# Optimization experiments

Hardware: AMD Instinct MI355X
Metric: run time of the kernel (lower is better)

The kernel has to match this reference:

```python
import jax, jax.numpy as jnp
import numpy as np
from jax import lax

BITS = 8

def dec2bin(q, bits=BITS):
    # q: integer-valued float tensor (NCHW or OIHW); stack two's-complement bit-planes along axis 1
    u = jnp.mod(jnp.round(q).astype(jnp.int32), 2 ** bits)
    return jnp.concatenate([((u >> k) & 1) for k in range(bits)], axis=1).astype(jnp.float32)

def quant_sym(x, bits=BITS):
    # brevitas-style signed symmetric per-tensor fake-quant (zero_point = 0)
    n = 2.0 ** (bits - 1) - 1.0
    scale = jnp.max(jnp.abs(x)) / n
    q = jnp.clip(jnp.round(x / scale), -n, n)  # q == value/scale + zero_point
    return q * scale, q

def quant_relu(x, bits=BITS):
    # QuantReLU: unsigned per-tensor fake-quant after relu
    r = jnp.maximum(x, 0.0)
    n = 2.0 ** bits - 1.0
    scale = jnp.max(r) / n
    q = jnp.clip(jnp.round(r / scale), 0.0, n)
    return q * scale, q

def conv(x, w, stride, pad):
    return lax.conv_general_dilated(x, w, (stride, stride), [(pad, pad), (pad, pad)],
                                    dimension_numbers=('NCHW', 'OIHW', 'NCHW'))

def bn(x, g, b, m, v, eps=1e-5):
    inv = g * lax.rsqrt(v + eps)
    return x * inv[None, :, None, None] + (b - m * inv)[None, :, None, None]

def setup_inputs() -> dict:
    key = jax.random.key(0)
    ks = jax.random.split(key, 11)
    N, C, H, W = 16, 64, 56, 56
    return {
        'x':  jax.random.normal(ks[0], (N, C, H, W), jnp.float32),
        'w1': jax.random.normal(ks[1], (C, C, 3, 3), jnp.float32) * 0.05,
        'w2': jax.random.normal(ks[2], (C, C, 3, 3), jnp.float32) * 0.05,
        'g1': jax.random.uniform(ks[3], (C,), jnp.float32, 0.5, 1.5),
        'b1': jax.random.normal(ks[4], (C,), jnp.float32) * 0.1,
        'm1': jax.random.normal(ks[5], (C,), jnp.float32) * 0.1,
        'v1': jax.random.uniform(ks[6], (C,), jnp.float32, 0.5, 1.5),
        'g2': jax.random.uniform(ks[7], (C,), jnp.float32, 0.5, 1.5),
        'b2': jax.random.normal(ks[8], (C,), jnp.float32) * 0.1,
        'm2': jax.random.normal(ks[9], (C,), jnp.float32) * 0.1,
        'v2': jax.random.uniform(ks[10], (C,), jnp.float32, 0.5, 1.5),
    }

def reference(x, w1, w2, g1, b1, m1, v1, g2, b2, m2, v2):
    stride = 1
    # quant_input (QuantIdentity) produces the quant tensor entering the block
    xq, qx = quant_sym(x)
    identity = xq
    # HM_activation: total number of set bits in the int activation
    HM_act = jnp.sum(dec2bin(qx))
    # HM_energy: L1 norm of conv over bit-decomposed int activations/weights
    w1q, qw1 = quant_sym(w1)
    HM_energy = jnp.sum(jnp.abs(conv(dec2bin(qx), dec2bin(qw1), stride, 1)))
    # conv1 -> bn1 -> QuantReLU
    o = bn(conv(xq, w1q, stride, 1), g1, b1, m1, v1)
    o1, q1 = quant_relu(o)
    HM_act = HM_act + jnp.sum(dec2bin(q1))
    w2q, qw2 = quant_sym(w2)
    HM_energy = HM_energy + jnp.sum(jnp.abs(conv(dec2bin(q1), dec2bin(qw2), 1, 1)))
    # conv2 -> bn2 -> residual add -> QuantReLU
    o = bn(conv(o1, w2q, 1, 1), g2, b2, m2, v2)
    o = o + identity
    out, _ = quant_relu(o)
    return out, HM_act, HM_energy
```

## Files before the change

kernel.cpp:

```cpp
#include <hip/hip_runtime.h>

using u32 = unsigned int;
typedef int v4i __attribute__((ext_vector_type(4)));

constexpr int N_IMG   = 16;
constexpr int PADROW  = 4096;
constexpr int ROWS_PI = 58;

constexpr size_t OFS_QX   = 4096;
constexpr size_t SZ_QPAD  = (size_t)(1 + N_IMG * ROWS_PI) * PADROW;
constexpr size_t OFS_Q1   = OFS_QX + SZ_QPAD;
constexpr size_t OFS_O1   = OFS_Q1 + SZ_QPAD;
constexpr size_t SZ_OF    = (size_t)N_IMG * 56 * 56 * 64 * 4;
constexpr size_t OFS_O2   = OFS_O1 + SZ_OF;
constexpr size_t OFS_QW1  = OFS_O2 + SZ_OF;
constexpr size_t OFS_QW2  = OFS_QW1 + 36864;
constexpr size_t OFS_WB1  = OFS_QW2 + 36864;
constexpr size_t OFS_WB2  = OFS_WB1 + 18432;
constexpr size_t OFS_WSUM = OFS_WB2 + 18432;
constexpr size_t OFS_SCAL = OFS_WSUM + 256;
constexpr size_t OFS_STX  = OFS_SCAL + 384;
constexpr size_t OFS_STQ  = OFS_STX + 18432;
constexpr size_t OFS_WSRED= OFS_STQ + 18432;
constexpr size_t WS_NEED  = OFS_WSRED + 4096;
constexpr size_t ZSPAN    = OFS_WSRED - OFS_WSUM;
constexpr size_t OUTN     = (size_t)16 * 64 * 56 * 56;

static __device__ __forceinline__ float block_redmax(float v, float* red, int t) {
    red[t] = v; __syncthreads();
    for (int s = 128; s > 0; s >>= 1) {
        if (t < s) red[t] = fmaxf(red[t], red[t + s]);
        __syncthreads();
    }
    float r = red[0]; __syncthreads();
    return r;
}

__global__ __launch_bounds__(256) void k_absmax_qw(const float* __restrict__ x,
                                                   const float* __restrict__ w1,
                                                   const float* __restrict__ w2,
                                                   char* __restrict__ qw1, char* __restrict__ qw2,
                                                   int* __restrict__ wb1, int* __restrict__ wb2,
                                                   int* __restrict__ wsum, float* __restrict__ scal,
                                                   float* __restrict__ wsred) {
    __shared__ union { float red[256]; int wsl[256]; } sm;
    int b = blockIdx.x, t = threadIdx.x;
    if (b < 1024) {
        float mx = 0.f;
        const float4* p4 = (const float4*)x;
        for (int i = b * 256 + t; i < 802816; i += 1024 * 256) {
            float4 v = p4[i];
            mx = fmaxf(mx, fmaxf(fmaxf(fabsf(v.x), fabsf(v.y)),
                                 fmaxf(fabsf(v.z), fabsf(v.w))));
        }
        mx = block_redmax(mx, sm.red, t);
        if (t == 0) wsred[b] = mx;
        return;
    }
    int wu = b - 1024;
    int wsel = wu / 9, kp = wu - wsel * 9;
    const float* w = wsel ? w2 : w1;
    char* qw = wsel ? qw2 : qw1;
    int* wb  = wsel ? wb2 : wb1;
    float mx = 0.f;
    const float4* p4 = (const float4*)w;
    for (int i = t; i < 9216; i += 256) {
        float4 v = p4[i];
        mx = fmaxf(mx, fmaxf(fmaxf(fabsf(v.x), fabsf(v.y)),
                             fmaxf(fabsf(v.z), fabsf(v.w))));
    }
    float maxW = block_redmax(mx, sm.red, t);
    if (t == 0 && kp == 0) scal[1 + wsel] = maxW;
    float s = maxW / 127.f;
    int co = t & 63, cg = t >> 6, ci0 = cg * 16;
    signed char qv[16];
    int qsum = 0;
#pragma unroll
    for (int i = 0; i < 16; i++) {
        int ci = ci0 + i;
        float v = w[((size_t)co * 64 + ci) * 9 + kp];
        float qf = rintf(v / s);
        qf = fminf(fmaxf(qf, -127.f), 127.f);
        int q = (int)qf;
        qv[i] = (signed char)q;
        qsum += q;
    }
    u32 pk[4];
#pragma unroll
    for (int d = 0; d < 4; d++)
        pk[d] = ((u32)(unsigned char)qv[d*4]) | ((u32)(unsigned char)qv[d*4+1] << 8)
              | ((u32)(unsigned char)qv[d*4+2] << 16) | ((u32)(unsigned char)qv[d*4+3] << 24);
    *(uint4*)&qw[(size_t)(kp * 64 + co) * 64 + ci0] = *(uint4*)pk;
#pragma unroll
    for (int i = 0; i < 16; i++) {
        u32 uu = (u32)(unsigned char)qv[i];
#pragma unroll
        for (int k = 0; k < 8; k++) {
            unsigned long long bal = __ballot((uu >> k) & 1);
            if (co == 0) wb[((ci0 + i) * 8 + k) * 9 + kp] = __popcll(bal);
        }
    }
    if (wsel == 1) {
        __syncthreads();
        sm.wsl[t] = qsum; __syncthreads();
        if (t < 64)
            atomicAdd(&wsum[t], sm.wsl[t] + sm.wsl[t + 64] + sm.wsl[t + 128] + sm.wsl[t + 192]);
    }
}

__global__ __launch_bounds__(256) void k_quant_x(const float* __restrict__ x,
                                                 char* __restrict__ qpad,
                                                 const float* __restrict__ wsred,
                                                 float* __restrict__ scal) {
    __shared__ union { float red[256]; char lq[4096]; } sm;
    int n = blockIdx.x, yy = blockIdx.y, t = threadIdx.x;
    u32* row = (u32*)(qpad + (size_t)(1 + n * ROWS_PI + yy) * PADROW);
    if (n == 0 && yy == 0) {
        u32* r0 = (u32*)qpad;
        for (int j = t; j < 1024; j += 256) r0[j] = 0u;
    }
    if (yy == 0 || yy == 57) {
        for (int j = t; j < 1024; j += 256) row[j] = 0u;
        return;
    }
    float a = fmaxf(fmaxf(wsred[t], wsred[t + 256]),
                    fmaxf(wsred[t + 512], wsred[t + 768]));
    float maxX = block_redmax(a, sm.red, t);
    if (n == 0 && yy == 1 && t == 0) scal[0] = maxX;
    int y = yy - 1;
    float sxq = maxX / 127.f;
    const float4* xr = (const float4*)(x + (size_t)n * 200704 + (size_t)y * 56);
    for (int j = t; j < 896; j += 256) {
        int c = j / 14, xq = j - c * 14;
        float4 v = xr[(size_t)c * 784 + xq];
#pragma unroll
        for (int i = 0; i < 4; i++) {
            float q = rintf(((const float*)&v)[i] / sxq);
            q = fminf(fmaxf(q, -127.f), 127.f);
            sm.lq[(4 * xq + i) * 64 + c] = (char)(int)q;
        }
    }
    __syncthreads();
    u32* lqd = (u32*)sm.lq;
    for (int j = t; j < 1024; j += 256) row[j] = (j < 896) ? lqd[j] : 0u;
}

static __device__ __forceinline__ void unpack_acc(u32 v, u32 pk[8]) {
#pragma unroll
    for (int k = 0; k < 8; k++) pk[k] += (v >> k) & 0x01010101u;
}

static __device__ __forceinline__ void reduce_cat(u32* red, int* gdst, const u32 pk[8],
                                                  bool active, int t) {
#pragma unroll
    for (int k = 0; k < 8; k++) red[t * 9 + k] = active ? pk[k] : 0u;
    __syncthreads();
#pragma unroll
    for (int p = t; p < 512; p += 256) {
        int ci = p >> 3, k = p & 7, ci4 = ci >> 2, bb = ci & 3;
        int sum = 0;
#pragma unroll
        for (int xo = 0; xo < 16; xo++)
            sum += (red[(xo * 16 + ci4) * 9 + k] >> (8 * bb)) & 0xFF;
        if (sum) atomicAdd(&gdst[p], sum);
    }
    __syncthreads();
}

template <int FROMF>
static __device__ __forceinline__ u32 pk_at(const u32* img, const float* ofb, float s1,
                                            u32 xm, int row, int xx, int ci4) {
    if (FROMF) {
        float4 v = *(const float4*)(ofb + (size_t)row * 3584 + xx * 64 + ci4 * 4);
        u32 pk = 0;
#pragma unroll
        for (int i = 0; i < 4; i++) {
            float vv = fmaxf(((const float*)&v)[i], 0.f);
            u32 q = (u32)(int)fminf(rintf(vv / s1), 255.f);
            pk |= q << (8 * i);
        }
        return pk;
    }
    return img[(size_t)row * 1024 + xx * 16 + ci4] ^ xm;
}

template <int FROMF>
static __device__ void stats_unit(u32* red, const char* qpad, const float* of, float s1,
                                  u32 xorm, int* gst, int s, int t) {
    int n = s >> 3, slab = s & 7;
    int ci4 = t & 15, xo = t >> 4;
    const u32* img = FROMF ? nullptr : (const u32*)(qpad + (size_t)(2 + n * ROWS_PI) * PADROW);
    const float* ofb = FROMF ? (of + (size_t)n * 56 * 3584) : nullptr;
    u32 xm = xorm * 0x01010101u;
    int y0 = slab * 7;
    {
        u32 pk[8] = {0,0,0,0,0,0,0,0};
#pragma unroll
        for (int r = 0; r < 7; r++)
#pragma unroll
            for (int j = 0; j < 4; j++) {
                int xx = xo + 16 * j;
                if (xx < 56) unpack_acc(pk_at<FROMF>(img, ofb, s1, xm, y0 + r, xx, ci4), pk);
            }
        reduce_cat(red, gst + 0 * 512, pk, true, t);
    }
    {
        u32 pk[8] = {0,0,0,0,0,0,0,0};
        bool act = (xo == 0);
        if (act)
#pragma unroll
            for (int r = 0; r < 7; r++)
                unpack_acc(pk_at<FROMF>(img, ofb, s1, xm, y0 + r, 0, ci4), pk);
        reduce_cat(red, gst + 3 * 512, pk, act, t);
    }
    {
        u32 pk[8] = {0,0,0,0,0,0,0,0};
        bool act = (xo == 7);
        if (act)
#pragma unroll
            for (int r = 0; r < 7; r++)
                unpack_acc(pk_at<FROMF>(img, ofb, s1, xm, y0 + r, 55, ci4), pk);
        reduce_cat(red, gst + 4 * 512, pk, act, t);
    }
    if (slab == 0) {
        u32 pk[8] = {0,0,0,0,0,0,0,0};
#pragma unroll
        for (int j = 0; j < 4; j++) {
            int xx = xo + 16 * j;
            if (xx < 56) unpack_acc(pk_at<FROMF>(img, ofb, s1, xm, 0, xx, ci4), pk);
        }
        reduce_cat(red, gst + 1 * 512, pk, true, t);
        if (t < 32) {
            int which = t >> 4, c4 = t & 15;
            u32 v = pk_at<FROMF>(img, ofb, s1, xm, 0, which ? 55 : 0, c4);
            for (int b = 0; b < 4; b++)
                for (int k = 0; k < 8; k++)
                    if ((v >> (8 * b + k)) & 1)
                        atomicAdd(&gst[(5 + which) * 512 + (c4 * 4 + b) * 8 + k], 1);
        }
    }
    if (slab == 7) {
        u32 pk[8] = {0,0,0,0,0,0,0,0};
#pragma unroll
        for (int j = 0; j < 4; j++) {
            int xx = xo + 16 * j;
            if (xx < 56) unpack_acc(pk_at<FROMF>(img, ofb, s1, xm, 55, xx, ci4), pk);
        }
        reduce_cat(red, gst + 2 * 512, pk, true, t);
        if (t < 32) {
            int which = t >> 4, c4 = t & 15;
            u32 v = pk_at<FROMF>(img, ofb, s1, xm, 55, which ? 55 : 0, c4);
            for (int b = 0; b < 4; b++)
                for (int k = 0; k < 8; k++)
                    if ((v >> (8 * b + k)) & 1)
                        atomicAdd(&gst[(7 + which) * 512 + (c4 * 4 + b) * 8 + k], 1);
        }
    }
}

template <int SECOND>
__global__ __launch_bounds__(256, 2) void k_conv(const char* __restrict__ qin,
                                                 const char* __restrict__ qw,
                                                 const int* __restrict__ wsum,
                                                 const char* __restrict__ qid,
                                                 const float* __restrict__ gg, const float* __restrict__ bb,
                                                 const float* __restrict__ mmp, const float* __restrict__ vvp,
                                                 const float* __restrict__ scal,
                                                 float* __restrict__ outp, u32* __restrict__ rmaxp) {
    __shared__ __align__(16) u32 lb[11520];
    __shared__ __align__(16) u32 lin[3960];
    __shared__ float red[4];
    int b = blockIdx.x, t = threadIdx.x;
    int w = t >> 6, lane = t & 63, mq = lane & 15, quad = lane >> 4;
    int u0 = b * 2;
    int n = u0 / 56, y = u0 - n * 56;
    const uint4* bq4 = (const uint4*)qw;
    for (int j4 = t; j4 < 2304; j4 += 256) {
        int r_ = j4 >> 2, rem = j4 & 3;
        *(uint4*)&lb[r_ * 20 + rem * 4] = bq4[j4];
    }
    const uint4* qin4 = (const uint4*)qin;
    size_t pbase = (size_t)(1 + n * ROWS_PI + y) * 256;
    for (int r4 = t; r4 < 792; r4 += 256) {
        int ky = r4 / 264, r = r4 - ky * 264;
        int px = r >> 2, rem = r & 3;
        *(uint4*)&lin[(ky * 66 + px) * 20 + rem * 4] = qin4[pbase + (size_t)ky * 256 - 4 + r];
    }
    float sIn = SECOND ? __uint_as_float(((const u32*)scal)[32]) / 255.f : scal[0] / 127.f;
    float sW  = scal[1 + SECOND] / 127.f;
    float sx  = scal[0] / 127.f;
    float alpha[4], beta[4]; int wofs[4];
#pragma unroll
    for (int nt = 0; nt < 4; nt++) {
        int co = nt * 16 + mq;
        float inv = gg[co] * rsqrtf(vvp[co] + 1e-5f);
        alpha[nt] = sIn * sW * inv;
        beta[nt]  = bb[co] - mmp[co] * inv;
        wofs[nt]  = SECOND ? (wsum[co] << 7) : 0;
    }
    __syncthreads();
    float lmax = 0.f;
#pragma unroll
    for (int rr = 0; rr < 2; rr++) {
        if (rr == 1) {
            __syncthreads();
            for (int r4 = t; r4 < 264; r4 += 256) {
                int px = r4 >> 2, rem = r4 & 3;
                *(uint4*)&lin[px * 20 + rem * 4] = qin4[pbase + 3 * 256 - 4 + r4];
            }
            __syncthreads();
        }
        v4i acc[4] = {{0,0,0,0},{0,0,0,0},{0,0,0,0},{0,0,0,0}};
#pragma unroll
        for (int ky = 0; ky < 3; ky++) {
            int slot = (ky + rr) % 3;
#pragma unroll
            for (int kx = 0; kx < 3; kx++) {
                int px = w * 16 + mq + kx;
                v4i a = *(const v4i*)&lin[(slot * 66 + px) * 20 + quad * 4];
                int tap = ky * 3 + kx;
#pragma unroll
                for (int nt = 0; nt < 4; nt++) {
                    int co = nt * 16 + mq;
                    v4i bf = *(const v4i*)&lb[(tap * 64 + co) * 20 + quad * 4];
                    acc[nt] = __builtin_amdgcn_mfma_i32_16x16x64_i8(a, bf, acc[nt], 0, 0, 0);
                }
            }
        }
        int uu = u0 + rr, yr = y + rr;
        size_t rowb = (size_t)uu * 3584;
        const signed char* idrow = SECOND
            ? (const signed char*)(qid + (size_t)(2 + n * ROWS_PI + yr) * PADROW) : nullptr;
#pragma unroll
        for (int nt = 0; nt < 4; nt++) {
            int co = nt * 16 + mq;
#pragma unroll
            for (int r = 0; r < 4; r++) {
                int xx = w * 16 + quad * 4 + r;
                if (xx < 56) {
                    float o = (float)(acc[nt][r] + wofs[nt]) * alpha[nt] + beta[nt];
                    if (SECOND) o += sx * (float)idrow[xx * 64 + co];
                    outp[rowb + xx * 64 + co] = o;
                    lmax = fmaxf(lmax, o);
                }
            }
        }
    }
#pragma unroll
    for (int off = 32; off > 0; off >>= 1) lmax = fmaxf(lmax, __shfl_down(lmax, off));
    if (lane == 0) red[w] = lmax;
    __syncthreads();
    if (t == 0)
        atomicMax(rmaxp, __float_as_uint(fmaxf(fmaxf(red[0], red[1]), fmaxf(red[2], red[3]))));
}

__global__ __launch_bounds__(256) void k_qrelu1(const float* __restrict__ o1,
                                                char* __restrict__ q1,
                                                const char* __restrict__ qx,
                                                const float* __restrict__ scal,
                                                int* __restrict__ stx, int* __restrict__ stq) {
    __shared__ u32 sred[2304];
    int b = blockIdx.x, t = threadIdx.x;
    if (b >= 1056) {
        float s1 = __uint_as_float(((const u32*)scal)[32]) / 255.f;
        stats_unit<1>(sred, nullptr, o1, s1, 0u, stq, b - 1056, t);
        return;
    }
    if (b >= 928) { stats_unit<0>(sred, qx, nullptr, 0.f, 0u, stx, b - 928, t); return; }
    int n = b / 58, yy = b - n * 58;
    u32* row = (u32*)(q1 + (size_t)(1 + n * ROWS_PI + yy) * PADROW);
    if (n == 0 && yy == 0) {
        u32* r0 = (u32*)q1;
        for (int j = t; j < 1024; j += 256) r0[j] = 0x80808080u;
    }
    if (yy == 0 || yy == 57) {
        for (int j = t; j < 1024; j += 256) row[j] = 0x80808080u;
        return;
    }
    int y = yy - 1;
    float s1 = __uint_as_float(((const u32*)scal)[32]) / 255.f;
    const float4* o4 = (const float4*)(o1 + (size_t)(n * 56 + y) * 3584);
    for (int j = t; j < 1024; j += 256) {
        u32 pk = 0x80808080u;
        if (j < 896) {
            float4 v = o4[j];
            pk = 0u;
#pragma unroll
            for (int i = 0; i < 4; i++) {
                float vv = fmaxf(((const float*)&v)[i], 0.f);
                float q = fminf(rintf(vv / s1), 255.f);
                pk |= ((u32)(unsigned char)(char)((int)q - 128)) << (8 * i);
            }
        }
        row[j] = pk;
    }
}

__global__ __launch_bounds__(256) void k_final(const float* __restrict__ o2,
                                               const float* __restrict__ scal,
                                               float* __restrict__ outp,
                                               const int* __restrict__ stx, const int* __restrict__ stq,
                                               const int* __restrict__ wb1, const int* __restrict__ wb2) {
    __shared__ union { float lt[64 * 57]; long long r1[256]; } sm;
    int b = blockIdx.x, t = threadIdx.x;
    if (b == 448) {
        long long act = 0, en = 0;
#pragma unroll
        for (int half = 0; half < 2; half++) {
            int tt = t + half * 256;
#pragma unroll
            for (int wsel = 0; wsel < 2; wsel++) {
                const int* st = wsel ? stq : stx;
                const int* wb = wsel ? wb2 : wb1;
                long long s[9];
#pragma unroll
                for (int j = 0; j < 9; j++) s[j] = st[j * 512 + tt];
                int wr[9];
#pragma unroll
                for (int j = 0; j < 9; j++) wr[j] = wb[tt * 9 + j];
                long long wall = 0;
#pragma unroll
                for (int j = 0; j < 9; j++) wall += wr[j];
                long long wr0 = (long long)wr[0] + wr[1] + wr[2];
                long long wr2 = (long long)wr[6] + wr[7] + wr[8];
                long long wc0 = (long long)wr[0] + wr[3] + wr[6];
                long long wc2 = (long long)wr[2] + wr[5] + wr[8];
                en += s[0] * wall - s[1] * wr2 - s[2] * wr0 - s[3] * wc2 - s[4] * wc0
                    + s[5] * (long long)wr[8] + s[6] * (long long)wr[6]
                    + s[7] * (long long)wr[2] + s[8] * (long long)wr[0];
                act += s[0];
            }
        }
        sm.r1[t] = en; __syncthreads();
        for (int s = 128; s > 0; s >>= 1) { if (t < s) sm.r1[t] += sm.r1[t + s]; __syncthreads(); }
        long long etot = sm.r1[0]; __syncthreads();
        sm.r1[t] = act; __syncthreads();
        for (int s = 128; s > 0; s >>= 1) { if (t < s) sm.r1[t] += sm.r1[t + s]; __syncthreads(); }
        if (t == 0) {
            outp[OUTN]     = (float)sm.r1[0];
            outp[OUTN + 1] = (float)etot;
        }
        return;
    }
    float s2 = __uint_as_float(((const u32*)scal)[64]) / 255.f;
#pragma unroll
    for (int rr = 0; rr < 2; rr++) {
        int u = b * 2 + rr;
        int n = u / 56, y = u - n * 56;
        __syncthreads();
        const float4* o4 = (const float4*)(o2 + (size_t)u * 3584);
        for (int j = t; j < 896; j += 256) {
            int xx = j >> 4, c4 = j & 15;
            float4 v = o4[j];
#pragma unroll
            for (int i = 0; i < 4; i++) {
                float vv = fmaxf(((const float*)&v)[i], 0.f);
                float q = fminf(rintf(vv / s2), 255.f);
                sm.lt[(4 * c4 + i) * 57 + xx] = q * s2;
            }
        }
        __syncthreads();
        for (int idx = t; idx < 3584; idx += 256) {
            int co = idx / 56, xx = idx - co * 56;
            outp[(size_t)n * 200704 + (size_t)co * 3136 + y * 56 + xx] = sm.lt[co * 57 + xx];
        }
    }
}

extern "C" void kernel_launch(void* const* d_in, const int* in_sizes, int n_in,
                              void* d_out, int out_size, void* d_ws, size_t ws_size,
                              hipStream_t stream) {
    if (ws_size < WS_NEED) return;
    const float* x  = (const float*)d_in[0];
    const float* w1 = (const float*)d_in[1];
    const float* w2 = (const float*)d_in[2];
    const float* g1 = (const float*)d_in[3];
    const float* b1 = (const float*)d_in[4];
    const float* m1 = (const float*)d_in[5];
    const float* v1 = (const float*)d_in[6];
    const float* g2 = (const float*)d_in[7];
    const float* b2 = (const float*)d_in[8];
    const float* m2 = (const float*)d_in[9];
    const float* v2 = (const float*)d_in[10];
    char* ws = (char*)d_ws;
    char* qx  = ws + OFS_QX;
    char* q1  = ws + OFS_Q1;
    float* o1 = (float*)(ws + OFS_O1);
    float* o2 = (float*)(ws + OFS_O2);
    char* qw1 = ws + OFS_QW1;
    char* qw2 = ws + OFS_QW2;
    int* wb1  = (int*)(ws + OFS_WB1);
    int* wb2  = (int*)(ws + OFS_WB2);
    int* wsum = (int*)(ws + OFS_WSUM);
    float* scal = (float*)(ws + OFS_SCAL);
    u32* rmax1 = (u32*)(ws + OFS_SCAL + 128);
    u32* rmax2 = (u32*)(ws + OFS_SCAL + 256);
    int* stx  = (int*)(ws + OFS_STX);
    int* stq  = (int*)(ws + OFS_STQ);
    float* wsred = (float*)(ws + OFS_WSRED);
    float* outp = (float*)d_out;

    (void)hipMemsetAsync(ws + OFS_WSUM, 0, ZSPAN, stream);
    k_absmax_qw<<<1042, 256, 0, stream>>>(x, w1, w2, qw1, qw2, wb1, wb2, wsum, scal, wsred);
    k_quant_x<<<dim3(16, 58), 256, 0, stream>>>(x, qx, wsred, scal);
    k_conv<0><<<448, 256, 0, stream>>>(qx, qw1, wsum, nullptr,
                                       g1, b1, m1, v1, scal, o1, rmax1);
    k_qrelu1<<<1184, 256, 0, stream>>>(o1, q1, qx, scal, stx, stq);
    k_conv<1><<<448, 256, 0, stream>>>(q1, qw2, wsum, qx,
                                       g2, b2, m2, v2, scal, o2, rmax2);
    k_final<<<449, 256, 0, stream>>>(o2, scal, outp, stx, stq, wb1, wb2);
}
```

Measured before the change: 174.3 us.

## Load conv operands directly from global memory instead of staging in LDS

The int8 conv kernel no longer stages weights and input rows in shared memory with barriers. Each wave now reads its MFMA A/B fragments straight from global memory, relying on L2/L1 caching, and handles both output rows in one tap loop with two accumulator sets. Weight fragments are reused across both rows. The absmax kernel's block order is also changed so the weight-quant blocks come first. This removes the LDS footprint and syncs, which may allow higher occupancy, but it makes every fragment load a global access and doubles the accumulator registers.

Result: no change. 176.1 us (+1.0%).

```diff
diff --git a/kernel.cpp b/kernel.cpp
--- a/kernel.cpp
+++ b/kernel.cpp
@@ -45,20 +45,20 @@
                                                    float* __restrict__ wsred) {
     __shared__ union { float red[256]; int wsl[256]; } sm;
     int b = blockIdx.x, t = threadIdx.x;
-    if (b < 1024) {
+    if (b >= 18) {
+        int xb = b - 18;
         float mx = 0.f;
         const float4* p4 = (const float4*)x;
-        for (int i = b * 256 + t; i < 802816; i += 1024 * 256) {
+        for (int i = xb * 256 + t; i < 802816; i += 1024 * 256) {
             float4 v = p4[i];
             mx = fmaxf(mx, fmaxf(fmaxf(fabsf(v.x), fabsf(v.y)),
                                  fmaxf(fabsf(v.z), fabsf(v.w))));
         }
         mx = block_redmax(mx, sm.red, t);
-        if (t == 0) wsred[b] = mx;
+        if (t == 0) wsred[xb] = mx;
         return;
     }
-    int wu = b - 1024;
-    int wsel = wu / 9, kp = wu - wsel * 9;
+    int wsel = b / 9, kp = b - wsel * 9;
     const float* w = wsel ? w2 : w1;
     char* qw = wsel ? qw2 : qw1;
     int* wb  = wsel ? wb2 : wb1;
@@ -267,24 +267,30 @@
                                                  const float* __restrict__ mmp, const float* __restrict__ vvp,
                                                  const float* __restrict__ scal,
                                                  float* __restrict__ outp, u32* __restrict__ rmaxp) {
-    __shared__ __align__(16) u32 lb[11520];
-    __shared__ __align__(16) u32 lin[3960];
     __shared__ float red[4];
     int b = blockIdx.x, t = threadIdx.x;
     int w = t >> 6, lane = t & 63, mq = lane & 15, quad = lane >> 4;
     int u0 = b * 2;
     int n = u0 / 56, y = u0 - n * 56;
-    const uint4* bq4 = (const uint4*)qw;
-    for (int j4 = t; j4 < 2304; j4 += 256) {
-        int r_ = j4 >> 2, rem = j4 & 3;
-        *(uint4*)&lb[r_ * 20 + rem * 4] = bq4[j4];
-    }
-    const uint4* qin4 = (const uint4*)qin;
-    size_t pbase = (size_t)(1 + n * ROWS_PI + y) * 256;
-    for (int r4 = t; r4 < 792; r4 += 256) {
-        int ky = r4 / 264, r = r4 - ky * 264;
-        int px = r >> 2, rem = r & 3;
-        *(uint4*)&lin[(ky * 66 + px) * 20 + rem * 4] = qin4[pbase + (size_t)ky * 256 - 4 + r];
+    const v4i* qin4 = (const v4i*)qin;
+    size_t rbase = (size_t)(1 + n * ROWS_PI + y) * 256;
+    v4i acc[2][4] = {{{0,0,0,0},{0,0,0,0},{0,0,0,0},{0,0,0,0}},
+                     {{0,0,0,0},{0,0,0,0},{0,0,0,0},{0,0,0,0}}};
+#pragma unroll
+    for (int tap = 0; tap < 9; tap++) {
+        const int ky = tap / 3, kx = tap - ky * 3;
+        v4i bf[4];
+#pragma unroll
+        for (int nt = 0; nt < 4; nt++)
+            bf[nt] = *(const v4i*)&qw[(size_t)((tap * 64 + nt * 16 + mq) << 6) + quad * 16];
+        int px = w * 16 + mq + kx;
+#pragma unroll
+        for (int rr = 0; rr < 2; rr++) {
+            v4i a = qin4[rbase + (size_t)(rr + ky) * 256 - 4 + px * 4 + quad];
+#pragma unroll
+            for (int nt = 0; nt < 4; nt++)
+                acc[rr][nt] = __builtin_amdgcn_mfma_i32_16x16x64_i8(a, bf[nt], acc[rr][nt], 0, 0, 0);
+        }
     }
     float sIn = SECOND ? __uint_as_float(((const u32*)scal)[32]) / 255.f : scal[0] / 127.f;
     float sW  = scal[1 + SECOND] / 127.f;
@@ -298,35 +304,9 @@
         beta[nt]  = bb[co] - mmp[co] * inv;
         wofs[nt]  = SECOND ? (wsum[co] << 7) : 0;
     }
-    __syncthreads();
     float lmax = 0.f;
 #pragma unroll
     for (int rr = 0; rr < 2; rr++) {
-        if (rr == 1) {
-            __syncthreads();
-            for (int r4 = t; r4 < 264; r4 += 256) {
-                int px = r4 >> 2, rem = r4 & 3;
-                *(uint4*)&lin[px * 20 + rem * 4] = qin4[pbase + 3 * 256 - 4 + r4];
-            }
-            __syncthreads();
-        }
-        v4i acc[4] = {{0,0,0,0},{0,0,0,0},{0,0,0,0},{0,0,0,0}};
-#pragma unroll
-        for (int ky = 0; ky < 3; ky++) {
-            int slot = (ky + rr) % 3;
-#pragma unroll
-            for (int kx = 0; kx < 3; kx++) {
-                int px = w * 16 + mq + kx;
-                v4i a = *(const v4i*)&lin[(slot * 66 + px) * 20 + quad * 4];
-                int tap = ky * 3 + kx;
-#pragma unroll
-                for (int nt = 0; nt < 4; nt++) {
-                    int co = nt * 16 + mq;
-                    v4i bf = *(const v4i*)&lb[(tap * 64 + co) * 20 + quad * 4];
-                    acc[nt] = __builtin_amdgcn_mfma_i32_16x16x64_i8(a, bf, acc[nt], 0, 0, 0);
-                }
-            }
-        }
         int uu = u0 + rr, yr = y + rr;
         size_t rowb = (size_t)uu * 3584;
         const signed char* idrow = SECOND
@@ -338,7 +318,7 @@
             for (int r = 0; r < 4; r++) {
                 int xx = w * 16 + quad * 4 + r;
                 if (xx < 56) {
-                    float o = (float)(acc[nt][r] + wofs[nt]) * alpha[nt] + beta[nt];
+                    float o = (float)(acc[rr][nt][r] + wofs[nt]) * alpha[nt] + beta[nt];
                     if (SECOND) o += sx * (float)idrow[xx * 64 + co];
                     outp[rowb + xx * 64 + co] = o;
                     lmax = fmaxf(lmax, o);
```
